# Kernel tuning notes

Hardware: AMD Instinct MI355X
Metric: run time of the kernel (lower is better)

Reference implementation:

```python
import jax, jax.numpy as jnp
import numpy as np
from jax import lax

GAMMA = 1.0
BIG = 1e8  # finite stand-in for +inf boundary (exp(-BIG/gamma) underflows to 0, so math is exact)


def _soft_dtw(x, y, gamma):
    """Soft-DTW values R[N, M] per batch element. x: (B,N,D), y: (B,M,D)."""
    B, N, _ = x.shape
    M = y.shape[1]
    # pairwise squared-L2 cost matrix (B, N, M)
    x2 = jnp.sum(x * x, axis=-1)  # (B, N)
    y2 = jnp.sum(y * y, axis=-1)  # (B, M)
    D = x2[:, :, None] + y2[:, None, :] - 2.0 * jnp.einsum('bnd,bmd->bnm', x, y)

    i = jnp.arange(N + 1)
    # R matrix diagonals, indexed by i (row); diag d holds R[i, d-i].
    r0 = jnp.full((B, N + 1), BIG, dtype=x.dtype).at[:, 0].set(0.0)  # d=0: R[0,0]=0
    r1 = jnp.full((B, N + 1), BIG, dtype=x.dtype)                    # d=1: boundaries

    def step(carry, d):
        r2, r1 = carry  # diagonals d-2 and d-1
        j = d - i
        valid = (i >= 1) & (i <= N) & (j >= 1) & (j <= M)
        ii = jnp.clip(i - 1, 0, N - 1)
        jj = jnp.clip(j - 1, 0, M - 1)
        cost = D[:, ii, jj]                                      # (B, N+1)
        pad = jnp.full((B, 1), BIG, dtype=x.dtype)
        r1_up = jnp.concatenate([pad, r1[:, :-1]], axis=1)       # R[i-1, j]
        r2_up = jnp.concatenate([pad, r2[:, :-1]], axis=1)       # R[i-1, j-1]
        stacked = jnp.stack([r1_up, r1, r2_up], axis=0)
        smin = -gamma * jax.scipy.special.logsumexp(-stacked / gamma, axis=0)
        new = jnp.where(valid[None, :], cost + smin, BIG)
        return (r1, new), None

    (_, r_last), _ = lax.scan(step, (r0, r1), jnp.arange(2, N + M + 1))
    return r_last[:, N]  # R[N, M] per batch


def setup_inputs() -> dict:
    key = jax.random.key(0)
    k1, k2 = jax.random.split(key)
    B, T, D = 64, 512, 64
    inputs = jax.random.normal(k1, (B, T, D), dtype=jnp.float32)
    targets = jax.random.normal(k2, (B, T, D), dtype=jnp.float32)
    return {"inputs": inputs, "targets": targets}


def reference(inputs, targets):
    # forward: mean over batch of soft-DTW(gamma=1.0) with pairwise squared-L2 cost
    return jnp.mean(_soft_dtw(inputs, targets, GAMMA))
```

## Files before the change

kernel.cpp:

```cpp
#include <hip/hip_runtime.h>

#define BIG 100000000.0f
constexpr int BATCH = 64;
constexpr int T = 512;
constexpr int DIMS = 64;

__global__ __launch_bounds__(256) void pairdist_kernel(
    const float* __restrict__ x, const float* __restrict__ y,
    float* __restrict__ D) {
  int bid = blockIdx.x;
  int b = bid >> 6;
  int tile = bid & 63;
  int n0 = (tile >> 3) << 6;
  int m0 = (tile & 7) << 6;

  __shared__ float xs[64][65];
  __shared__ float ys[64][65];
  __shared__ float x2s[64], y2s[64];

  const float* xb = x + ((size_t)b * T + n0) * DIMS;
  const float* yb = y + ((size_t)b * T + m0) * DIMS;
  int tid = threadIdx.x;

  for (int e = tid; e < 64 * 64; e += 256) {
    int r = e >> 6, c = e & 63;
    xs[r][c] = xb[(size_t)r * DIMS + c];
    ys[r][c] = yb[(size_t)r * DIMS + c];
  }
  __syncthreads();

  if (tid < 64) {
    float s = 0.f;
    #pragma unroll
    for (int k = 0; k < 64; ++k) { float v = xs[tid][k]; s += v * v; }
    x2s[tid] = s;
  } else if (tid < 128) {
    int r = tid - 64;
    float s = 0.f;
    #pragma unroll
    for (int k = 0; k < 64; ++k) { float v = ys[r][k]; s += v * v; }
    y2s[r] = s;
  }
  __syncthreads();

  int tr = tid >> 4, tc = tid & 15;
  int r0 = tr * 4, c0 = tc * 4;
  float acc[4][4] = {};
  #pragma unroll 8
  for (int k = 0; k < 64; ++k) {
    float a0 = xs[r0 + 0][k], a1 = xs[r0 + 1][k];
    float a2 = xs[r0 + 2][k], a3 = xs[r0 + 3][k];
    float b0 = ys[c0 + 0][k], b1 = ys[c0 + 1][k];
    float b2 = ys[c0 + 2][k], b3 = ys[c0 + 3][k];
    acc[0][0] += a0 * b0; acc[0][1] += a0 * b1; acc[0][2] += a0 * b2; acc[0][3] += a0 * b3;
    acc[1][0] += a1 * b0; acc[1][1] += a1 * b1; acc[1][2] += a1 * b2; acc[1][3] += a1 * b3;
    acc[2][0] += a2 * b0; acc[2][1] += a2 * b1; acc[2][2] += a2 * b2; acc[2][3] += a2 * b3;
    acc[3][0] += a3 * b0; acc[3][1] += a3 * b1; acc[3][2] += a3 * b2; acc[3][3] += a3 * b3;
  }

  #pragma unroll
  for (int r = 0; r < 4; ++r) {
    float4 v;
    float xn = x2s[r0 + r];
    v.x = xn + y2s[c0 + 0] - 2.f * acc[r][0];
    v.y = xn + y2s[c0 + 1] - 2.f * acc[r][1];
    v.z = xn + y2s[c0 + 2] - 2.f * acc[r][2];
    v.w = xn + y2s[c0 + 3] - 2.f * acc[r][3];
    *(float4*)&D[(((size_t)b * T) + (n0 + r0 + r)) * T + (m0 + c0)] = v;
  }
}

__global__ __launch_bounds__(512) void dp_kernel(const float* __restrict__ D,
                                                 float* __restrict__ out) {
  int b = blockIdx.x;
  int tid = threadIdx.x;
  int i = tid + 1;

  __shared__ float rbuf[3][T + 1];
  for (int e = tid; e < 3 * (T + 1); e += 512) ((float*)rbuf)[e] = BIG;
  __syncthreads();
  if (tid == 0) rbuf[0][0] = 0.f;
  __syncthreads();

  float* rp2 = rbuf[0];
  float* rp1 = rbuf[1];
  float* rc  = rbuf[2];

  const float* Db = D + (size_t)b * T * T + (size_t)(i - 1) * T;

  float cost_next;
  {
    int j = 2 - i;
    int jj = min(max(j, 1), T) - 1;
    cost_next = Db[jj];
  }

  float val = BIG;
  for (int d = 2; d <= 2 * T; ++d) {
    float cost = cost_next;
    {
      int jn = d + 1 - i;
      int jjn = min(max(jn, 1), T) - 1;
      cost_next = Db[jjn];
    }
    int j = d - i;
    float a = rp1[i - 1];
    float bb = rp1[i];
    float c = rp2[i - 1];
    float m = fminf(fminf(a, bb), c);
    float s = __expf(m - a) + __expf(m - bb) + __expf(m - c);
    val = (j >= 1 && j <= T) ? (cost + m - __logf(s)) : BIG;
    rc[i] = val;
    if (tid == 0) rc[0] = BIG;
    __syncthreads();
    float* tmp = rp2; rp2 = rp1; rp1 = rc; rc = tmp;
  }

  if (tid == T - 1) atomicAdd(out, val * (1.0f / BATCH));
}

__global__ __launch_bounds__(512) void dp_onfly_kernel(
    const float* __restrict__ x, const float* __restrict__ y,
    float* __restrict__ out) {
  int b = blockIdx.x;
  int tid = threadIdx.x;
  int i = tid + 1;

  __shared__ float ys[T][DIMS + 1];
  __shared__ float y2s[T];
  __shared__ float rbuf[3][T + 1];

  const float* yb = y + (size_t)b * T * DIMS;
  for (int e = tid; e < T * DIMS; e += 512) {
    int r = e >> 6, c = e & 63;
    ys[r][c] = yb[e];
  }
  for (int e = tid; e < 3 * (T + 1); e += 512) ((float*)rbuf)[e] = BIG;
  __syncthreads();
  if (tid == 0) rbuf[0][0] = 0.f;
  {
    float s = 0.f;
    #pragma unroll
    for (int k = 0; k < DIMS; ++k) { float v = ys[tid][k]; s += v * v; }
    y2s[tid] = s;
  }

  float xr[DIMS];
  float x2 = 0.f;
  const float* xb = x + ((size_t)b * T + (i - 1)) * DIMS;
  #pragma unroll
  for (int k = 0; k < DIMS; ++k) { xr[k] = xb[k]; x2 += xr[k] * xr[k]; }
  __syncthreads();

  float* rp2 = rbuf[0];
  float* rp1 = rbuf[1];
  float* rc  = rbuf[2];

  float val = BIG;
  for (int d = 2; d <= 2 * T; ++d) {
    int j = d - i;
    bool valid = (j >= 1) && (j <= T);
    float cost = 0.f;
    if (valid) {
      float dot = 0.f;
      #pragma unroll
      for (int k = 0; k < DIMS; ++k) dot += xr[k] * ys[j - 1][k];
      cost = x2 + y2s[j - 1] - 2.f * dot;
    }
    float a = rp1[i - 1];
    float bb = rp1[i];
    float c = rp2[i - 1];
    float m = fminf(fminf(a, bb), c);
    float s = __expf(m - a) + __expf(m - bb) + __expf(m - c);
    val = valid ? (cost + m - __logf(s)) : BIG;
    rc[i] = val;
    if (tid == 0) rc[0] = BIG;
    __syncthreads();
    float* tmp = rp2; rp2 = rp1; rp1 = rc; rc = tmp;
  }

  if (tid == T - 1) atomicAdd(out, val * (1.0f / BATCH));
}

extern "C" void kernel_launch(void* const* d_in, const int* in_sizes, int n_in,
                              void* d_out, int out_size, void* d_ws, size_t ws_size,
                              hipStream_t stream) {
  const float* x = (const float*)d_in[0];
  const float* y = (const float*)d_in[1];
  float* out = (float*)d_out;

  hipMemsetAsync(d_out, 0, sizeof(float), stream);

  size_t needD = (size_t)BATCH * T * T * sizeof(float);
  if (ws_size >= needD) {
    float* Dw = (float*)d_ws;
    pairdist_kernel<<<BATCH * 64, 256, 0, stream>>>(x, y, Dw);
    dp_kernel<<<BATCH, 512, 0, stream>>>(Dw, out);
  } else {
    dp_onfly_kernel<<<BATCH, 512, 0, stream>>>(x, y, out);
  }
}
```

Measured before the change: 430.1 us.

## Store cost matrix in anti-diagonal order and run DP in one wavefront

The pairwise-distance kernel now writes the cost matrix in anti-diagonal-major order, pre-scaled by log2(e). This lets the DP read each diagonal contiguously. The DP kernel now uses a single 64-lane wavefront per batch element with 8 values per lane held in registers. Neighbour values move between lanes through ds_bpermute instead of shared memory plus a block-wide barrier on every diagonal. Softmin uses base-2 exp/log intrinsics with min/med3/max to save one exp, and cost loads are prefetched three diagonals ahead. The trade-off is far fewer threads per batch (64 instead of 512), more serial work per lane, and scattered writes in the distance kernel.

```diff
diff --git a/kernel.cpp b/kernel.cpp
--- a/kernel.cpp
+++ b/kernel.cpp
@@ -1,11 +1,24 @@
 #include <hip/hip_runtime.h>
 
-#define BIG 100000000.0f
+#define BIGF 100000000.0f
+#define LOG2E 1.4426950408889634f
+#define LN2f 0.6931471805599453f
 constexpr int BATCH = 64;
 constexpr int T = 512;
 constexpr int DIMS = 64;
 
-__global__ __launch_bounds__(256) void pairdist_kernel(
+#if __has_builtin(__builtin_amdgcn_exp2f)
+#define EXP2F(x) __builtin_amdgcn_exp2f(x)
+#else
+#define EXP2F(x) __expf((x) * LN2f)
+#endif
+#if __has_builtin(__builtin_amdgcn_logf)
+#define LOG2F(x) __builtin_amdgcn_logf(x)
+#else
+#define LOG2F(x) (__logf(x) * LOG2E)
+#endif
+
+__global__ __launch_bounds__(256) void pairdist_diag_kernel(
     const float* __restrict__ x, const float* __restrict__ y,
     float* __restrict__ D) {
   int bid = blockIdx.x;
@@ -16,6 +29,7 @@
 
   __shared__ float xs[64][65];
   __shared__ float ys[64][65];
+  __shared__ float stage[64][66];
   __shared__ float x2s[64], y2s[64];
 
   const float* xb = x + ((size_t)b * T + n0) * DIMS;
@@ -60,63 +74,117 @@
 
   #pragma unroll
   for (int r = 0; r < 4; ++r) {
-    float4 v;
     float xn = x2s[r0 + r];
-    v.x = xn + y2s[c0 + 0] - 2.f * acc[r][0];
-    v.y = xn + y2s[c0 + 1] - 2.f * acc[r][1];
-    v.z = xn + y2s[c0 + 2] - 2.f * acc[r][2];
-    v.w = xn + y2s[c0 + 3] - 2.f * acc[r][3];
-    *(float4*)&D[(((size_t)b * T) + (n0 + r0 + r)) * T + (m0 + c0)] = v;
-  }
-}
-
-__global__ __launch_bounds__(512) void dp_kernel(const float* __restrict__ D,
-                                                 float* __restrict__ out) {
-  int b = blockIdx.x;
-  int tid = threadIdx.x;
-  int i = tid + 1;
-
-  __shared__ float rbuf[3][T + 1];
-  for (int e = tid; e < 3 * (T + 1); e += 512) ((float*)rbuf)[e] = BIG;
-  __syncthreads();
-  if (tid == 0) rbuf[0][0] = 0.f;
-  __syncthreads();
-
-  float* rp2 = rbuf[0];
-  float* rp1 = rbuf[1];
-  float* rc  = rbuf[2];
-
-  const float* Db = D + (size_t)b * T * T + (size_t)(i - 1) * T;
-
-  float cost_next;
-  {
-    int j = 2 - i;
-    int jj = min(max(j, 1), T) - 1;
-    cost_next = Db[jj];
-  }
-
-  float val = BIG;
-  for (int d = 2; d <= 2 * T; ++d) {
-    float cost = cost_next;
-    {
-      int jn = d + 1 - i;
-      int jjn = min(max(jn, 1), T) - 1;
-      cost_next = Db[jjn];
+    #pragma unroll
+    for (int c = 0; c < 4; ++c)
+      stage[r0 + r][c0 + c] = (xn + y2s[c0 + c] - 2.f * acc[r][c]) * LOG2E;
+  }
+  __syncthreads();
+
+  float* Dp = D + (size_t)b * (T * T);
+  int sub = tid >> 6, p = tid & 63;
+  #pragma unroll 1
+  for (int t4 = 0; t4 < 128; t4 += 4) {
+    int t = t4 + sub;
+    int rlo = (t > 63) ? t - 63 : 0;
+    int rhi = (t < 63) ? t : 63;
+    int r = rlo + p;
+    if (t <= 126 && r <= rhi) {
+      int c = t - r;
+      int i = n0 + r + 1;
+      int d = n0 + m0 + t + 2;
+      int lo = (d <= T + 1) ? 1 : d - T;
+      int off = (d <= T + 1) ? (((d - 2) * (d - 1)) >> 1)
+                             : (T * T - (((2 * T + 1 - d) * (2 * T + 2 - d)) >> 1));
+      Dp[off + (i - lo)] = stage[r][c];
     }
-    int j = d - i;
-    float a = rp1[i - 1];
-    float bb = rp1[i];
-    float c = rp2[i - 1];
-    float m = fminf(fminf(a, bb), c);
-    float s = __expf(m - a) + __expf(m - bb) + __expf(m - c);
-    val = (j >= 1 && j <= T) ? (cost + m - __logf(s)) : BIG;
-    rc[i] = val;
-    if (tid == 0) rc[0] = BIG;
-    __syncthreads();
-    float* tmp = rp2; rp2 = rp1; rp1 = rc; rc = tmp;
-  }
-
-  if (tid == T - 1) atomicAdd(out, val * (1.0f / BATCH));
+  }
+}
+
+#define LOADDIAG(CARR, dp_)                                                   \
+  if ((dp_) <= 2 * T) {                                                       \
+    const int lop  = ((dp_) <= T + 1) ? 1 : (dp_) - T;                        \
+    const int hip2 = ((dp_) - 1 < T) ? (dp_) - 1 : T;                         \
+    const int klop = (lop - 1) >> 6;                                          \
+    const int khip = (hip2 - 1) >> 6;                                         \
+    const int offp = ((dp_) <= T + 1)                                         \
+        ? ((((dp_) - 2) * ((dp_) - 1)) >> 1)                                  \
+        : (T * T - (((2 * T + 1 - (dp_)) * (2 * T + 2 - (dp_))) >> 1));       \
+    const float* Dr = Db + offp - lop;                                        \
+    _Pragma("unroll")                                                         \
+    for (int k = 0; k < 8; ++k)                                               \
+      if (k >= klop && k <= khip) CARR[k] = Dr[(k << 6) + lane + 1];          \
+  }
+
+#define STEP(dd_, RP2, RP1, ROUT, CARR)                                       \
+  {                                                                           \
+    const int dd  = (dd_);                                                    \
+    const int lo  = (dd <= T + 1) ? 1 : dd - T;                               \
+    const int hi  = (dd - 1 < T) ? dd - 1 : T;                                \
+    const int klo = (lo - 1) >> 6;                                            \
+    const int khi = (hi - 1) >> 6;                                            \
+    const int krot = (klo > 0) ? klo - 1 : 0;                                 \
+    float rot1[8], rot2[8];                                                   \
+    _Pragma("unroll")                                                         \
+    for (int k = 0; k < 8; ++k)                                               \
+      if (k >= krot && k <= khi) {                                            \
+        rot1[k] = __int_as_float(__builtin_amdgcn_ds_bpermute(                \
+            rot_addr, __float_as_int(RP1[k])));                               \
+        rot2[k] = __int_as_float(__builtin_amdgcn_ds_bpermute(                \
+            rot_addr, __float_as_int(RP2[k])));                               \
+      }                                                                       \
+    const float dzero = (dd == 2) ? 0.0f : BIGF;                              \
+    _Pragma("unroll")                                                         \
+    for (int k = 0; k < 8; ++k)                                               \
+      if (k >= klo && k <= khi) {                                             \
+        const int i = (k << 6) + lane + 1;                                    \
+        float up, dg;                                                         \
+        if (k == 0) {                                                         \
+          up = (lane == 0) ? BIGF : rot1[0];                                  \
+          dg = (lane == 0) ? dzero : rot2[0];                                 \
+        } else {                                                              \
+          up = (lane == 0) ? rot1[k - 1] : rot1[k];                           \
+          dg = (lane == 0) ? rot2[k - 1] : rot2[k];                           \
+        }                                                                     \
+        const float lf = RP1[k];                                              \
+        const float mn = fminf(fminf(up, lf), dg);                            \
+        const float md = __builtin_amdgcn_fmed3f(up, lf, dg);                 \
+        const float mx = fmaxf(fmaxf(up, lf), dg);                            \
+        const float s  = 1.0f + EXP2F(mn - md) + EXP2F(mn - mx);              \
+        const float val = CARR[k] + mn - LOG2F(s);                            \
+        const unsigned ju = (unsigned)(dd - i - 1);                           \
+        ROUT[k] = (ju < (unsigned)T) ? val : BIGF;                            \
+      }                                                                       \
+    LOADDIAG(CARR, dd + 3)                                                    \
+  }
+
+__global__ __launch_bounds__(64) void dp_diag_kernel(const float* __restrict__ D,
+                                                     float* __restrict__ out) {
+  const int b = blockIdx.x;
+  const int lane = threadIdx.x;
+  const float* __restrict__ Db = D + (size_t)b * (T * T);
+  const int rot_addr = ((lane + 63) & 63) << 2;
+
+  float A[8], Bv[8], C[8];
+  float cA[8], cB[8], cC[8];
+  #pragma unroll
+  for (int k = 0; k < 8; ++k) {
+    A[k] = BIGF; Bv[k] = BIGF; C[k] = BIGF;
+    cA[k] = 0.f; cB[k] = 0.f; cC[k] = 0.f;
+  }
+
+  LOADDIAG(cA, 2)
+  LOADDIAG(cB, 3)
+  LOADDIAG(cC, 4)
+
+  #pragma unroll 1
+  for (int d0 = 2; d0 <= 2 * T; d0 += 3) {
+    STEP(d0,     A,  Bv, C,  cA)
+    STEP(d0 + 1, Bv, C,  A,  cB)
+    STEP(d0 + 2, C,  A,  Bv, cC)
+  }
+
+  if (lane == 63) atomicAdd(out, Bv[7] * (LN2f / BATCH));
 }
 
 __global__ __launch_bounds__(512) void dp_onfly_kernel(
@@ -135,7 +203,7 @@
     int r = e >> 6, c = e & 63;
     ys[r][c] = yb[e];
   }
-  for (int e = tid; e < 3 * (T + 1); e += 512) ((float*)rbuf)[e] = BIG;
+  for (int e = tid; e < 3 * (T + 1); e += 512) ((float*)rbuf)[e] = BIGF;
   __syncthreads();
   if (tid == 0) rbuf[0][0] = 0.f;
   {
@@ -156,7 +224,7 @@
   float* rp1 = rbuf[1];
   float* rc  = rbuf[2];
 
-  float val = BIG;
+  float val = BIGF;
   for (int d = 2; d <= 2 * T; ++d) {
     int j = d - i;
     bool valid = (j >= 1) && (j <= T);
@@ -172,9 +240,9 @@
     float c = rp2[i - 1];
     float m = fminf(fminf(a, bb), c);
     float s = __expf(m - a) + __expf(m - bb) + __expf(m - c);
-    val = valid ? (cost + m - __logf(s)) : BIG;
+    val = valid ? (cost + m - __logf(s)) : BIGF;
     rc[i] = val;
-    if (tid == 0) rc[0] = BIG;
+    if (tid == 0) rc[0] = BIGF;
     __syncthreads();
     float* tmp = rp2; rp2 = rp1; rp1 = rc; rc = tmp;
   }
@@ -194,8 +262,8 @@
   size_t needD = (size_t)BATCH * T * T * sizeof(float);
   if (ws_size >= needD) {
     float* Dw = (float*)d_ws;
-    pairdist_kernel<<<BATCH * 64, 256, 0, stream>>>(x, y, Dw);
-    dp_kernel<<<BATCH, 512, 0, stream>>>(Dw, out);
+    pairdist_diag_kernel<<<BATCH * 64, 256, 0, stream>>>(x, y, Dw);
+    dp_diag_kernel<<<BATCH, 64, 0, stream>>>(Dw, out);
   } else {
     dp_onfly_kernel<<<BATCH, 512, 0, stream>>>(x, y, out);
   }
```

Result: slower. 859.2 us (+99.8%).
